# Performance work log

Measured on AMD Instinct MI355X. Metric: run time of the kernel, lower is better.

Reference implementation:

```python
import jax, jax.numpy as jnp
import numpy as np

F_DIM, HID, H, DQ, DV = 1024, 4096, 16, 64, 64
EPS = 1e-6

def layer_norm(x, w, b):
    mu = jnp.mean(x, axis=-1, keepdims=True)
    var = jnp.mean(jnp.square(x - mu), axis=-1, keepdims=True)
    return (x - mu) * jax.lax.rsqrt(var + EPS) * w + b

def setup_inputs() -> dict:
    key = jax.random.key(0)
    ks = jax.random.split(key, 8)
    s = 0.02
    return {
        'x': jax.random.normal(ks[0], (4, 2048, F_DIM), dtype=jnp.float32),
        'ln1_w': jnp.ones((F_DIM,), jnp.float32),
        'ln1_b': jnp.zeros((F_DIM,), jnp.float32),
        'wq_w': jax.random.normal(ks[1], (H * DQ, F_DIM), jnp.float32) * s,
        'wq_b': jnp.zeros((H * DQ,), jnp.float32),
        'wk_w': jax.random.normal(ks[2], (H * DQ, F_DIM), jnp.float32) * s,
        'wk_b': jnp.zeros((H * DQ,), jnp.float32),
        'wv_w': jax.random.normal(ks[3], (H * DV, F_DIM), jnp.float32) * s,
        'wv_b': jnp.zeros((H * DV,), jnp.float32),
        'fc_w': jax.random.normal(ks[4], (F_DIM, H * DV), jnp.float32) * s,
        'fc_b': jnp.zeros((F_DIM,), jnp.float32),
        'ln2_w': jnp.ones((F_DIM,), jnp.float32),
        'ln2_b': jnp.zeros((F_DIM,), jnp.float32),
        'fc1_w': jax.random.normal(ks[5], (HID, F_DIM), jnp.float32) * s,
        'fc1_b': jnp.zeros((HID,), jnp.float32),
        'fc2_w': jax.random.normal(ks[6], (F_DIM, HID), jnp.float32) * s,
        'fc2_b': jnp.zeros((F_DIM,), jnp.float32),
    }

def reference(x, ln1_w, ln1_b, wq_w, wq_b, wk_w, wk_b, wv_w, wv_b,
              fc_w, fc_b, ln2_w, ln2_b, fc1_w, fc1_b, fc2_w, fc2_b):
    B, S, _ = x.shape
    # --- pre-LN multi-head self-attention ---
    h = layer_norm(x, ln1_w, ln1_b)
    q = (h @ wq_w.T + wq_b).reshape(B, S, H, DQ).transpose(0, 2, 1, 3)  # [B,H,S,dq]
    k = (h @ wk_w.T + wk_b).reshape(B, S, H, DQ).transpose(0, 2, 1, 3)
    v = (h @ wv_w.T + wv_b).reshape(B, S, H, DV).transpose(0, 2, 1, 3)
    attn = jax.nn.softmax(jnp.einsum('bhqd,bhkd->bhqk', q, k) / jnp.sqrt(jnp.float32(DQ)), axis=-1)
    out = jnp.einsum('bhqk,bhkd->bhqd', attn, v).transpose(0, 2, 1, 3).reshape(B, S, H * DV)
    x = x + (out @ fc_w.T + fc_b)
    # --- pre-LN residual MLP ---
    h2 = layer_norm(x, ln2_w, ln2_b)
    ff = jax.nn.relu(h2 @ fc1_w.T + fc1_b) @ fc2_w.T + fc2_b
    return x + ff
```

## Files before the change

kernel.cpp:

```cpp
#include <hip/hip_runtime.h>

#define F_DIMC 1024
#define HIDC   4096
#define NH     16
#define SEQ    2048
#define BATCH  4
#define ROWS   (BATCH * SEQ)
#define MEG    (1u << 20)
#define QSCALE 0.18033688011112042f

typedef unsigned short u16t;
typedef __attribute__((ext_vector_type(8))) short short8;
typedef __attribute__((ext_vector_type(4))) float floatx4;
typedef __attribute__((address_space(1))) void gvoid_t;
typedef __attribute__((address_space(3))) void lvoid_t;
#define ASYNC16(g, l) __builtin_amdgcn_global_load_lds((gvoid_t*)(g), (lvoid_t*)(l), 16, 0, 0)

#if __has_builtin(__builtin_amdgcn_exp2f)
#define EXP2(x) __builtin_amdgcn_exp2f(x)
#else
#define EXP2(x) exp2f(x)
#endif

__device__ __forceinline__ u16t f2bf(float f) {
    union { float f; unsigned u; } v; v.f = f;
    unsigned r = v.u + 0x7fffu + ((v.u >> 16) & 1u);
    return (u16t)(r >> 16);
}
__device__ __forceinline__ unsigned fasu(float f) {
    union { float f; unsigned u; } v; v.f = f; return v.u;
}

__global__ __launch_bounds__(256) void ln_kernel(const float* __restrict__ x,
                                                 const float* __restrict__ w,
                                                 const float* __restrict__ b,
                                                 u16t* __restrict__ out) {
    const int row = blockIdx.x;
    const int t = threadIdx.x;
    const float* xp = x + (size_t)row * F_DIMC;

    float4 v = *(const float4*)(xp + t * 4);
    float s  = v.x + v.y + v.z + v.w;
    float ss = v.x * v.x + v.y * v.y + v.z * v.z + v.w * v.w;
    for (int off = 32; off; off >>= 1) {
        s  += __shfl_down(s, off);
        ss += __shfl_down(ss, off);
    }
    __shared__ float red[8];
    const int wid = t >> 6, lid = t & 63;
    if (lid == 0) { red[wid] = s; red[4 + wid] = ss; }
    __syncthreads();
    if (t == 0) {
        float S  = red[0] + red[1] + red[2] + red[3];
        float SS = red[4] + red[5] + red[6] + red[7];
        float mu  = S * (1.0f / F_DIMC);
        float var = SS * (1.0f / F_DIMC) - mu * mu;
        red[0] = mu;
        red[1] = rsqrtf(var + 1e-6f);
    }
    __syncthreads();
    const float mu = red[0], rs = red[1];

    float4 wv = *(const float4*)(w + t * 4);
    float4 bv = *(const float4*)(b + t * 4);
    ushort4 o = make_ushort4(f2bf((v.x - mu) * rs * wv.x + bv.x),
                             f2bf((v.y - mu) * rs * wv.y + bv.y),
                             f2bf((v.z - mu) * rs * wv.z + bv.z),
                             f2bf((v.w - mu) * rs * wv.w + bv.w));
    *(ushort4*)(out + (size_t)row * F_DIMC + t * 4) = o;
}

__global__ __launch_bounds__(256) void wconv_kernel(const float* __restrict__ w0,
        const float* __restrict__ w1, const float* __restrict__ w2,
        const float* __restrict__ w3, const float* __restrict__ w4,
        const float* __restrict__ w5, u16t* __restrict__ dst) {
    const size_t e = ((size_t)blockIdx.x * 256 + threadIdx.x) * 4;
    const float* src; size_t off;
    if      (e < 1 * MEG) { src = w0; off = e; }
    else if (e < 2 * MEG) { src = w1; off = e - 1 * MEG; }
    else if (e < 3 * MEG) { src = w2; off = e - 2 * MEG; }
    else if (e < 4 * MEG) { src = w3; off = e - 3 * MEG; }
    else if (e < 8 * MEG) { src = w4; off = e - 4 * MEG; }
    else                  { src = w5; off = e - 8 * MEG; }
    float4 f = *(const float4*)(src + off);
    *(ushort4*)(dst + e) = make_ushort4(f2bf(f.x), f2bf(f.y), f2bf(f.z), f2bf(f.w));
}

#define DP_PROLOGUE_AND_LOOP(Aq, Wq, Kdim, NBX)                                \
    __shared__ u16t As[2][256 * 64] __attribute__((aligned(16)));              \
    __shared__ u16t Ws[2][128 * 64] __attribute__((aligned(16)));              \
    const int t = threadIdx.x;                                                 \
    const int lane = t & 63;                                                   \
    const int wave = t >> 6;                                                   \
    const int wm = wave >> 1, wn = wave & 1;                                   \
    const int fm = lane & 15, fq = lane >> 4;                                  \
    const int l7 = lane & 7;                                                   \
         \
    const int nwg = gridDim.x;                                                 \
    const int swzb = (blockIdx.x & 7) * (nwg >> 3) + (blockIdx.x >> 3);        \
    const int m0 = (swzb / (NBX)) * 256, n0 = (swzb % (NBX)) * 128;            \
               \
    const u16t* ag[4]; const u16t* wg2[2];                                     \
    int alo[4]; int wlo[2];                                                    \
    _Pragma("unroll")                                                          \
    for (int i = 0; i < 4; ++i) {                                              \
        const int beta = i * 512 + t;                                          \
        const int r = beta >> 3, j = (beta & 7) ^ (r & 7);                     \
        ag[i] = (Aq) + (size_t)(m0 + r) * (Kdim) + j * 8;                      \
        alo[i] = beta * 8;                                                     \
    }                                                                          \
    _Pragma("unroll")                                                          \
    for (int i = 0; i < 2; ++i) {                                              \
        const int beta = i * 512 + t;                                          \
        const int r = beta >> 3, j = (beta & 7) ^ (r & 7);                     \
        wg2[i] = (Wq) + (size_t)(n0 + r) * (Kdim) + j * 8;                     \
        wlo[i] = beta * 8;                                                     \
    }                                                                          \
          \
    int abase[2], bbase[2];                                                    \
    _Pragma("unroll")                                                          \
    for (int ks = 0; ks < 2; ++ks) {                                           \
        const int sw = (ks * 4 + fq) ^ l7;                                     \
        abase[ks] = (wm * 64 + fm) * 64 + sw * 8;                              \
        bbase[ks] = (wn * 64 + fm) * 64 + sw * 8;                              \
    }                                                                          \
    const int NT = (Kdim) / 64;                                                \
                       \
    _Pragma("unroll")                                                          \
    for (int i = 0; i < 4; ++i) ASYNC16(ag[i], &As[0][alo[i]]);                \
    _Pragma("unroll")                                                          \
    for (int i = 0; i < 2; ++i) ASYNC16(wg2[i], &Ws[0][wlo[i]]);               \
    _Pragma("unroll")                                                          \
    for (int i = 0; i < 4; ++i) ASYNC16(ag[i] + 64, &As[1][alo[i]]);           \
    _Pragma("unroll")                                                          \
    for (int i = 0; i < 2; ++i) ASYNC16(wg2[i] + 64, &Ws[1][wlo[i]]);          \
    _Pragma("unroll")                                                          \
    for (int i = 0; i < 4; ++i) ag[i] += 128;                                  \
    _Pragma("unroll")                                                          \
    for (int i = 0; i < 2; ++i) wg2[i] += 128;                                 \
    asm volatile("s_waitcnt vmcnt(6)" ::: "memory");         \
    __builtin_amdgcn_s_barrier();                                              \
    __builtin_amdgcn_sched_barrier(0);                                         \
    floatx4 acc[4][4] = {};                                                    \
    for (int tt = 0; tt < NT; ++tt) {                                          \
        const u16t* Ab = As[tt & 1];                                           \
        const u16t* Wb = Ws[tt & 1];                                           \
                                      \
        short8 fa[4], fb[4];                                                   \
        _Pragma("unroll")                                                      \
        for (int mi = 0; mi < 4; ++mi)                                         \
            fa[mi] = *(const short8*)(Ab + abase[0] + mi * 1024);              \
        _Pragma("unroll")                                                      \
        for (int ni = 0; ni < 4; ++ni)                                         \
            fb[ni] = *(const short8*)(Wb + bbase[0] + ni * 1024);              \
        __builtin_amdgcn_s_setprio(1);                                         \
        _Pragma("unroll")                                                      \
        for (int mi = 0; mi < 4; ++mi)                                         \
            _Pragma("unroll")                                                  \
            for (int ni = 0; ni < 4; ++ni)                                     \
                acc[mi][ni] = __builtin_amdgcn_mfma_f32_16x16x32_bf16(         \
                    fa[mi], fb[ni], acc[mi][ni], 0, 0, 0);                     \
        __builtin_amdgcn_s_setprio(0);                                         \
                     \
        short8 fa1[4], fb1[4];                                                 \
        _Pragma("unroll")                                                      \
        for (int mi = 0; mi < 4; ++mi)                                         \
            fa1[mi] = *(const short8*)(Ab + abase[1] + mi * 1024);             \
        _Pragma("unroll")                                                      \
        for (int ni = 0; ni < 4; ++ni)                                         \
            fb1[ni] = *(const short8*)(Wb + bbase[1] + ni * 1024);             \
        asm volatile("s_waitcnt lgkmcnt(0)" ::: "memory");  \
        __builtin_amdgcn_s_barrier();        \
        __builtin_amdgcn_sched_barrier(0);                                     \
        if (tt + 2 < NT) {                                                     \
            const int pb = tt & 1;           \
            _Pragma("unroll")                                                  \
            for (int i = 0; i < 4; ++i) {                                      \
                ASYNC16(ag[i], &As[pb][alo[i]]); ag[i] += 64;                  \
            }                                                                  \
            _Pragma("unroll")                                                  \
            for (int i = 0; i < 2; ++i) {                                      \
                ASYNC16(wg2[i], &Ws[pb][wlo[i]]); wg2[i] += 64;                \
            }                                                                  \
                  \
            asm volatile("s_waitcnt vmcnt(6)" ::: "memory");                   \
        } else {                                                               \
            asm volatile("s_waitcnt vmcnt(0)" ::: "memory");                   \
        }                                                                      \
        __builtin_amdgcn_s_barrier();                                          \
        __builtin_amdgcn_sched_barrier(0);                                     \
              \
        __builtin_amdgcn_s_setprio(1);                                         \
        _Pragma("unroll")                                                      \
        for (int mi = 0; mi < 4; ++mi)                                         \
            _Pragma("unroll")                                                  \
            for (int ni = 0; ni < 4; ++ni)                                     \
                acc[mi][ni] = __builtin_amdgcn_mfma_f32_16x16x32_bf16(         \
                    fa1[mi], fb1[ni], acc[mi][ni], 0, 0, 0);                   \
        __builtin_amdgcn_s_setprio(0);                                         \
    }

template <bool RELU, bool RES, bool BF16OUT>
__global__ __launch_bounds__(512, 2) void gemm_dp(const u16t* __restrict__ A,
                                                  const u16t* __restrict__ W,
                                                  const float* __restrict__ bias,
                                                  const float* res, void* Cout,
                                                  int N, int K) {
    DP_PROLOGUE_AND_LOOP(A, W, K, N / 128)
    float bl[4];
#pragma unroll
    for (int ni = 0; ni < 4; ++ni) bl[ni] = bias[n0 + wn * 64 + ni * 16 + fm];
#pragma unroll
    for (int mi = 0; mi < 4; ++mi) {
#pragma unroll
        for (int ni = 0; ni < 4; ++ni) {
            const int col = n0 + wn * 64 + ni * 16 + fm;
#pragma unroll
            for (int r = 0; r < 4; ++r) {
                const int row = m0 + wm * 64 + mi * 16 + fq * 4 + r;
                const size_t off = (size_t)row * N + col;
                float c = acc[mi][ni][r] + bl[ni];
                if (RELU) c = fmaxf(c, 0.0f);
                if (RES)  c += res[off];
                if (BF16OUT) ((u16t*)Cout)[off] = f2bf(c);
                else         ((float*)Cout)[off] = c;
            }
        }
    }
}

__global__ __launch_bounds__(512, 2) void gemm_qkv(const u16t* __restrict__ A,
        const u16t* __restrict__ W,
        const float* __restrict__ wq_b, const float* __restrict__ wk_b,
        const float* __restrict__ wv_b,
        u16t* __restrict__ qb, u16t* __restrict__ kb, u16t* __restrict__ vtb) {
    DP_PROLOGUE_AND_LOOP(A, W, F_DIMC, 3072 / 128)
    const int which = n0 >> 10;
    const int nb = n0 & 1023;
    const float* bias = which == 0 ? wq_b : which == 1 ? wk_b : wv_b;
    float bl[4];
#pragma unroll
    for (int ni = 0; ni < 4; ++ni) bl[ni] = bias[nb + wn * 64 + ni * 16 + fm];

    if (which == 2) {
#pragma unroll
        for (int mi = 0; mi < 4; ++mi)
#pragma unroll
            for (int ni = 0; ni < 4; ++ni) {
                const int col = nb + wn * 64 + ni * 16 + fm;
                const int row0 = m0 + wm * 64 + mi * 16 + fq * 4;
                ushort4 pk = make_ushort4(f2bf(acc[mi][ni][0] + bl[ni]),
                                          f2bf(acc[mi][ni][1] + bl[ni]),
                                          f2bf(acc[mi][ni][2] + bl[ni]),
                                          f2bf(acc[mi][ni][3] + bl[ni]));
                *(ushort4*)(vtb + (size_t)col * ROWS + row0) = pk;
            }
    } else {
        u16t* dst = (which == 0) ? qb : kb;
        const float sc = (which == 0) ? QSCALE : 1.0f;
#pragma unroll
        for (int mi = 0; mi < 4; ++mi)
#pragma unroll
            for (int ni = 0; ni < 4; ++ni) {
                const int col = nb + wn * 64 + ni * 16 + fm;
#pragma unroll
                for (int r = 0; r < 4; ++r) {
                    const int row = m0 + wm * 64 + mi * 16 + fq * 4 + r;
                    dst[(size_t)row * F_DIMC + col] = f2bf((acc[mi][ni][r] + bl[ni]) * sc);
                }
            }
    }
}

__global__ __launch_bounds__(256, 4) void attn_mfma(const u16t* __restrict__ qb,
        const u16t* __restrict__ kbuf, const u16t* __restrict__ vtb,
        u16t* __restrict__ ab) {
    __shared__ u16t Kt[2][64 * 64] __attribute__((aligned(16)));
    __shared__ u16t Vs[64 * 64] __attribute__((aligned(16)));
    __shared__ u16t QP[128 * 64] __attribute__((aligned(16)));

    const int t = threadIdx.x;
    const int lane = t & 63;
    const int wave = t >> 6;
    const int l15 = lane & 15, q4 = lane >> 4;
    const int q0 = blockIdx.x * 128;
    const int bh = blockIdx.y;
    const int b = bh >> 4, hh = bh & 15;

#pragma unroll
    for (int c = 0; c < 4; ++c) {
        const int beta = c * 256 + t;
        const int r = beta >> 3, o = (beta & 7) ^ (r & 7);
        ASYNC16(qb + (size_t)(b * SEQ + q0 + r) * F_DIMC + hh * 64 + o * 8,
                QP + beta * 8);
    }
    const u16t* kg = kbuf + (size_t)(b * SEQ) * F_DIMC + hh * 64;
    const u16t* vg = vtb + (size_t)(hh * 64) * ROWS + b * SEQ;

    const int sb0 = t, sb1 = t + 256;
    const int sr0 = sb0 >> 3, so0 = (sb0 & 7) ^ (sr0 & 7);
    const int sr1 = sb1 >> 3, so1 = (sb1 & 7) ^ (sr1 & 7);
    const u16t* kp0 = kg + (size_t)sr0 * F_DIMC + so0 * 8;
    const u16t* kp1 = kg + (size_t)sr1 * F_DIMC + so1 * 8;
    const u16t* vp0 = vg + (size_t)sr0 * ROWS + so0 * 8;
    const u16t* vp1 = vg + (size_t)sr1 * ROWS + so1 * 8;

    ASYNC16(kp0, Kt[0] + sb0 * 8);
    ASYNC16(kp1, Kt[0] + sb1 * 8);
    ASYNC16(vp0, Vs + sb0 * 8);
    ASYNC16(vp1, Vs + sb1 * 8);
    kp0 += 64 * F_DIMC; kp1 += 64 * F_DIMC; vp0 += 64; vp1 += 64;
    __syncthreads();

    short8 fqr[2][2];
#pragma unroll
    for (int mt = 0; mt < 2; ++mt)
#pragma unroll
        for (int ks = 0; ks < 2; ++ks) {
            const int m = wave * 32 + mt * 16 + l15;
            const int oct = ks * 4 + q4;
            fqr[mt][ks] = *(const short8*)(QP + (m * 8 + (oct ^ (m & 7))) * 8);
        }

    short8 ones;
#pragma unroll
    for (int i = 0; i < 8; ++i) ones[i] = (short)0x3F80;

    floatx4 oacc[2][4] = {};
    floatx4 lacc[2] = {};

    for (int it = 0; it < SEQ / 64; ++it) {
        if (it + 1 < SEQ / 64) {
            u16t* kd = Kt[(it + 1) & 1];
            ASYNC16(kp0, kd + sb0 * 8);
            ASYNC16(kp1, kd + sb1 * 8);
            kp0 += 64 * F_DIMC; kp1 += 64 * F_DIMC;
        }
        const u16t* kcur = Kt[it & 1];

        short8 fk[4][2];
#pragma unroll
        for (int nt = 0; nt < 4; ++nt)
#pragma unroll
            for (int ks = 0; ks < 2; ++ks) {
                const int kr = nt * 16 + l15;
                const int oct = ks * 4 + q4;
                fk[nt][ks] = *(const short8*)(kcur + (kr * 8 + (oct ^ (kr & 7))) * 8);
            }
        floatx4 st[2][4] = {};
#pragma unroll
        for (int mt = 0; mt < 2; ++mt)
#pragma unroll
            for (int nt = 0; nt < 4; ++nt) {
                st[mt][nt] = __builtin_amdgcn_mfma_f32_16x16x32_bf16(
                    fk[nt][0], fqr[mt][0], st[mt][nt], 0, 0, 0);
                st[mt][nt] = __builtin_amdgcn_mfma_f32_16x16x32_bf16(
                    fk[nt][1], fqr[mt][1], st[mt][nt], 0, 0, 0);
            }

#pragma unroll
        for (int mt = 0; mt < 2; ++mt)
#pragma unroll
            for (int nt = 0; nt < 4; ++nt) {
                const float p0 = EXP2(st[mt][nt][0]);
                const float p1 = EXP2(st[mt][nt][1]);
                const float p2 = EXP2(st[mt][nt][2]);
                const float p3 = EXP2(st[mt][nt][3]);
                const unsigned lo = __builtin_amdgcn_perm(fasu(p1), fasu(p0), 0x07060302u);
                const unsigned hi = __builtin_amdgcn_perm(fasu(p3), fasu(p2), 0x07060302u);
                const int m = wave * 32 + mt * 16 + l15;
                const int logb = nt * 2 + (q4 >> 1);
                *(uint2*)(QP + (m * 8 + (logb ^ (m & 7))) * 8 + (q4 & 1) * 4) =
                    make_uint2(lo, hi);
            }

        __syncthreads();

        short8 fp[2][2], fv[4][2];
#pragma unroll
        for (int mt = 0; mt < 2; ++mt)
#pragma unroll
            for (int ks = 0; ks < 2; ++ks) {
                const int m = wave * 32 + mt * 16 + l15;
                const int oct = ks * 4 + q4;
                fp[mt][ks] = *(const short8*)(QP + (m * 8 + (oct ^ (m & 7))) * 8);
            }
#pragma unroll
        for (int nd = 0; nd < 4; ++nd)
#pragma unroll
            for (int ks = 0; ks < 2; ++ks) {
                const int d = nd * 16 + l15;
                const int oct = ks * 4 + q4;
                fv[nd][ks] = *(const short8*)(Vs + (d * 8 + (oct ^ (d & 7))) * 8);
            }
#pragma unroll
        for (int mt = 0; mt < 2; ++mt) {
#pragma unroll
            for (int nd = 0; nd < 4; ++nd) {
                oacc[mt][nd] = __builtin_amdgcn_mfma_f32_16x16x32_bf16(
                    fp[mt][0], fv[nd][0], oacc[mt][nd], 0, 0, 0);
                oacc[mt][nd] = __builtin_amdgcn_mfma_f32_16x16x32_bf16(
                    fp[mt][1], fv[nd][1], oacc[mt][nd], 0, 0, 0);
            }
            lacc[mt] = __builtin_amdgcn_mfma_f32_16x16x32_bf16(
                fp[mt][0], ones, lacc[mt], 0, 0, 0);
            lacc[mt] = __builtin_amdgcn_mfma_f32_16x16x32_bf16(
                fp[mt][1], ones, lacc[mt], 0, 0, 0);
        }

        __syncthreads();
        if (it + 1 < SEQ / 64) {
            ASYNC16(vp0, Vs + sb0 * 8);
            ASYNC16(vp1, Vs + sb1 * 8);
            vp0 += 64; vp1 += 64;
        }
    }

#pragma unroll
    for (int mt = 0; mt < 2; ++mt) {
        floatx4 rinv;
#pragma unroll
        for (int r = 0; r < 4; ++r) rinv[r] = 1.0f / lacc[mt][r];
#pragma unroll
        for (int nd = 0; nd < 4; ++nd)
#pragma unroll
            for (int r = 0; r < 4; ++r) {
                const int row = b * SEQ + q0 + wave * 32 + mt * 16 + q4 * 4 + r;
                const int col = hh * 64 + nd * 16 + l15;
                ab[(size_t)row * F_DIMC + col] = f2bf(oacc[mt][nd][r] * rinv[r]);
            }
    }
}

extern "C" void kernel_launch(void* const* d_in, const int* in_sizes, int n_in,
                              void* d_out, int out_size, void* d_ws, size_t ws_size,
                              hipStream_t stream) {
    const float* x     = (const float*)d_in[0];
    const float* ln1_w = (const float*)d_in[1];
    const float* ln1_b = (const float*)d_in[2];
    const float* wq_w  = (const float*)d_in[3];
    const float* wq_b  = (const float*)d_in[4];
    const float* wk_w  = (const float*)d_in[5];
    const float* wk_b  = (const float*)d_in[6];
    const float* wv_w  = (const float*)d_in[7];
    const float* wv_b  = (const float*)d_in[8];
    const float* fc_w  = (const float*)d_in[9];
    const float* fc_b  = (const float*)d_in[10];
    const float* ln2_w = (const float*)d_in[11];
    const float* ln2_b = (const float*)d_in[12];
    const float* fc1_w = (const float*)d_in[13];
    const float* fc1_b = (const float*)d_in[14];
    const float* fc2_w = (const float*)d_in[15];
    const float* fc2_b = (const float*)d_in[16];

    float* out = (float*)d_out;
    u16t*  ws  = (u16t*)d_ws;

    u16t* wbuf = ws;
    u16t* bwqkv = wbuf;
    u16t* bwfc = wbuf + 3 * MEG;
    u16t* bwf1 = wbuf + 4 * MEG;
    u16t* bwf2 = wbuf + 8 * MEG;
    u16t* h    = wbuf + 12 * MEG;
    u16t* qb   = h + 8 * MEG;
    u16t* kb   = qb + 8 * MEG;
    u16t* vtb  = kb + 8 * MEG;
    u16t* ab   = vtb + 8 * MEG;
    u16t* ff   = qb;

    const dim3 blk(256);
    const dim3 blk512(512);
    const int gQKV = (ROWS / 256) * (3072 / 128);
    const int gF   = (ROWS / 256) * (F_DIMC / 128);
    const int gH   = (ROWS / 256) * (HIDC / 128);

    wconv_kernel<<<12 * MEG / 1024, blk, 0, stream>>>(wq_w, wk_w, wv_w, fc_w, fc1_w, fc2_w, wbuf);
    ln_kernel<<<ROWS, blk, 0, stream>>>(x, ln1_w, ln1_b, h);
    gemm_qkv<<<gQKV, blk512, 0, stream>>>(h, bwqkv, wq_b, wk_b, wv_b, qb, kb, vtb);
    attn_mfma<<<dim3(SEQ / 128, BATCH * NH), blk, 0, stream>>>(qb, kb, vtb, ab);
    gemm_dp<false, true, false><<<gF, blk512, 0, stream>>>(ab, bwfc, fc_b, x, out, F_DIMC, F_DIMC);
    ln_kernel<<<ROWS, blk, 0, stream>>>(out, ln2_w, ln2_b, h);
    gemm_dp<true, false, true><<<gH, blk512, 0, stream>>>(h, bwf1, fc1_b, nullptr, ff, HIDC, F_DIMC);
    gemm_dp<false, true, false><<<gF, blk512, 0, stream>>>(ff, bwf2, fc2_b, out, out, F_DIMC, HIDC);
}
```

Measured before the change: 514.7 us.

## Triple-buffer GEMM LDS stages, flip tile to 128x256, drop a barrier

Rewrites the shared GEMM core to use a three-stage LDS ring instead of double buffering. The global-to-LDS prefetch for tile tt+2 is issued at the start of each iteration rather than after a mid-iteration barrier. Both k-halves of the fragments are read up front, which removes one workgroup barrier per k-step. The block tile changes from 256x128 to 128x256 with a 2x4 wave layout, and the block-to-tile mapping changes so consecutive blocks walk along M. The cost is more LDS per block (about 144 KB), which leaves little room under the LDS limit, and a different L2 reuse pattern.

```diff
diff --git a/kernel.cpp b/kernel.cpp
--- a/kernel.cpp
+++ b/kernel.cpp
@@ -86,110 +86,97 @@
     *(ushort4*)(dst + e) = make_ushort4(f2bf(f.x), f2bf(f.y), f2bf(f.z), f2bf(f.w));
 }
 
-#define DP_PROLOGUE_AND_LOOP(Aq, Wq, Kdim, NBX)                                \
-    __shared__ u16t As[2][256 * 64] __attribute__((aligned(16)));              \
-    __shared__ u16t Ws[2][128 * 64] __attribute__((aligned(16)));              \
+#define DP_CORE(Aq, Wq, Kdim)                                                  \
+    __shared__ u16t As[3][128 * 64] __attribute__((aligned(16)));              \
+    __shared__ u16t Bs[3][256 * 64] __attribute__((aligned(16)));              \
     const int t = threadIdx.x;                                                 \
     const int lane = t & 63;                                                   \
     const int wave = t >> 6;                                                   \
-    const int wm = wave >> 1, wn = wave & 1;                                   \
+    const int wm = wave >> 2, wn = wave & 3;                                   \
     const int fm = lane & 15, fq = lane >> 4;                                  \
-    const int l7 = lane & 7;                                                   \
-         \
+        \
     const int nwg = gridDim.x;                                                 \
     const int swzb = (blockIdx.x & 7) * (nwg >> 3) + (blockIdx.x >> 3);        \
-    const int m0 = (swzb / (NBX)) * 256, n0 = (swzb % (NBX)) * 128;            \
-               \
-    const u16t* ag[4]; const u16t* wg2[2];                                     \
-    int alo[4]; int wlo[2];                                                    \
-    _Pragma("unroll")                                                          \
-    for (int i = 0; i < 4; ++i) {                                              \
+    const int m0 = (swzb & 63) * 128;                \
+    const int n0 = (swzb >> 6) * 256;                                          \
+                \
+    const u16t* ag[2]; int alo[2];                                             \
+    _Pragma("unroll")                                                          \
+    for (int i = 0; i < 2; ++i) {                                              \
         const int beta = i * 512 + t;                                          \
         const int r = beta >> 3, j = (beta & 7) ^ (r & 7);                     \
         ag[i] = (Aq) + (size_t)(m0 + r) * (Kdim) + j * 8;                      \
         alo[i] = beta * 8;                                                     \
     }                                                                          \
-    _Pragma("unroll")                                                          \
-    for (int i = 0; i < 2; ++i) {                                              \
+    const u16t* bg[4]; int blo[4];                                             \
+    _Pragma("unroll")                                                          \
+    for (int i = 0; i < 4; ++i) {                                              \
         const int beta = i * 512 + t;                                          \
         const int r = beta >> 3, j = (beta & 7) ^ (r & 7);                     \
-        wg2[i] = (Wq) + (size_t)(n0 + r) * (Kdim) + j * 8;                     \
-        wlo[i] = beta * 8;                                                     \
+        bg[i] = (Wq) + (size_t)(n0 + r) * (Kdim) + j * 8;                      \
+        blo[i] = beta * 8;                                                     \
     }                                                                          \
-          \
-    int abase[2], bbase[2];                                                    \
-    _Pragma("unroll")                                                          \
-    for (int ks = 0; ks < 2; ++ks) {                                           \
-        const int sw = (ks * 4 + fq) ^ l7;                                     \
-        abase[ks] = (wm * 64 + fm) * 64 + sw * 8;                              \
-        bbase[ks] = (wn * 64 + fm) * 64 + sw * 8;                              \
+                \
+    int aoffk[2], boffk[2];                                                    \
+    {                                                                          \
+        const int ra0 = wm * 64 + fm, rb0 = wn * 64 + fm;                      \
+        _Pragma("unroll")                                                      \
+        for (int ks = 0; ks < 2; ++ks) {                                       \
+            aoffk[ks] = ra0 * 64 + ((ks * 4 + fq) ^ (ra0 & 7)) * 8;            \
+            boffk[ks] = rb0 * 64 + ((ks * 4 + fq) ^ (rb0 & 7)) * 8;            \
+        }                                                                      \
     }                                                                          \
     const int NT = (Kdim) / 64;                                                \
                        \
     _Pragma("unroll")                                                          \
-    for (int i = 0; i < 4; ++i) ASYNC16(ag[i], &As[0][alo[i]]);                \
-    _Pragma("unroll")                                                          \
-    for (int i = 0; i < 2; ++i) ASYNC16(wg2[i], &Ws[0][wlo[i]]);               \
-    _Pragma("unroll")                                                          \
-    for (int i = 0; i < 4; ++i) ASYNC16(ag[i] + 64, &As[1][alo[i]]);           \
-    _Pragma("unroll")                                                          \
-    for (int i = 0; i < 2; ++i) ASYNC16(wg2[i] + 64, &Ws[1][wlo[i]]);          \
-    _Pragma("unroll")                                                          \
-    for (int i = 0; i < 4; ++i) ag[i] += 128;                                  \
-    _Pragma("unroll")                                                          \
-    for (int i = 0; i < 2; ++i) wg2[i] += 128;                                 \
+    for (int i = 0; i < 2; ++i) ASYNC16(ag[i], &As[0][alo[i]]);                \
+    _Pragma("unroll")                                                          \
+    for (int i = 0; i < 4; ++i) ASYNC16(bg[i], &Bs[0][blo[i]]);                \
+    _Pragma("unroll")                                                          \
+    for (int i = 0; i < 2; ++i) { ASYNC16(ag[i] + 64, &As[1][alo[i]]); ag[i] += 128; } \
+    _Pragma("unroll")                                                          \
+    for (int i = 0; i < 4; ++i) { ASYNC16(bg[i] + 64, &Bs[1][blo[i]]); bg[i] += 128; } \
     asm volatile("s_waitcnt vmcnt(6)" ::: "memory");         \
     __builtin_amdgcn_s_barrier();                                              \
     __builtin_amdgcn_sched_barrier(0);                                         \
     floatx4 acc[4][4] = {};                                                    \
+    int sc = 0, ss = 2;                                                        \
     for (int tt = 0; tt < NT; ++tt) {                                          \
-        const u16t* Ab = As[tt & 1];                                           \
-        const u16t* Wb = Ws[tt & 1];                                           \
-                                      \
-        short8 fa[4], fb[4];                                                   \
-        _Pragma("unroll")                                                      \
-        for (int mi = 0; mi < 4; ++mi)                                         \
-            fa[mi] = *(const short8*)(Ab + abase[0] + mi * 1024);              \
-        _Pragma("unroll")                                                      \
-        for (int ni = 0; ni < 4; ++ni)                                         \
-            fb[ni] = *(const short8*)(Wb + bbase[0] + ni * 1024);              \
+        const u16t* Ab = As[sc];                                               \
+        const u16t* Bb = Bs[sc];                                               \
+        if (tt + 2 < NT) {                \
+            u16t* la = As[ss]; u16t* lb = Bs[ss];                              \
+            _Pragma("unroll")                                                  \
+            for (int i = 0; i < 2; ++i) { ASYNC16(ag[i], la + alo[i]); ag[i] += 64; } \
+            _Pragma("unroll")                                                  \
+            for (int i = 0; i < 4; ++i) { ASYNC16(bg[i], lb + blo[i]); bg[i] += 64; } \
+        }                                                                      \
+        short8 fb0[4], fa0[4], fb1[4], fa1[4];                                 \
+        _Pragma("unroll")                                                      \
+        for (int ni = 0; ni < 4; ++ni) fb0[ni] = *(const short8*)(Bb + boffk[0] + ni * 1024); \
+        _Pragma("unroll")                                                      \
+        for (int mi = 0; mi < 4; ++mi) fa0[mi] = *(const short8*)(Ab + aoffk[0] + mi * 1024); \
+        _Pragma("unroll")                                                      \
+        for (int ni = 0; ni < 4; ++ni) fb1[ni] = *(const short8*)(Bb + boffk[1] + ni * 1024); \
+        _Pragma("unroll")                                                      \
+        for (int mi = 0; mi < 4; ++mi) fa1[mi] = *(const short8*)(Ab + aoffk[1] + mi * 1024); \
+        asm volatile("s_waitcnt lgkmcnt(8)" ::: "memory");   \
+        __builtin_amdgcn_sched_barrier(0);                                     \
         __builtin_amdgcn_s_setprio(1);                                         \
         _Pragma("unroll")                                                      \
         for (int mi = 0; mi < 4; ++mi)                                         \
             _Pragma("unroll")                                                  \
             for (int ni = 0; ni < 4; ++ni)                                     \
                 acc[mi][ni] = __builtin_amdgcn_mfma_f32_16x16x32_bf16(         \
-                    fa[mi], fb[ni], acc[mi][ni], 0, 0, 0);                     \
+                    fa0[mi], fb0[ni], acc[mi][ni], 0, 0, 0);                   \
         __builtin_amdgcn_s_setprio(0);                                         \
-                     \
-        short8 fa1[4], fb1[4];                                                 \
-        _Pragma("unroll")                                                      \
-        for (int mi = 0; mi < 4; ++mi)                                         \
-            fa1[mi] = *(const short8*)(Ab + abase[1] + mi * 1024);             \
-        _Pragma("unroll")                                                      \
-        for (int ni = 0; ni < 4; ++ni)                                         \
-            fb1[ni] = *(const short8*)(Wb + bbase[1] + ni * 1024);             \
-        asm volatile("s_waitcnt lgkmcnt(0)" ::: "memory");  \
-        __builtin_amdgcn_s_barrier();        \
+        asm volatile("s_waitcnt lgkmcnt(0)" ::: "memory");   \
         __builtin_amdgcn_sched_barrier(0);                                     \
-        if (tt + 2 < NT) {                                                     \
-            const int pb = tt & 1;           \
-            _Pragma("unroll")                                                  \
-            for (int i = 0; i < 4; ++i) {                                      \
-                ASYNC16(ag[i], &As[pb][alo[i]]); ag[i] += 64;                  \
-            }                                                                  \
-            _Pragma("unroll")                                                  \
-            for (int i = 0; i < 2; ++i) {                                      \
-                ASYNC16(wg2[i], &Ws[pb][wlo[i]]); wg2[i] += 64;                \
-            }                                                                  \
-                  \
-            asm volatile("s_waitcnt vmcnt(6)" ::: "memory");                   \
-        } else {                                                               \
-            asm volatile("s_waitcnt vmcnt(0)" ::: "memory");                   \
-        }                                                                      \
+                                       \
+        if (tt + 2 < NT) { asm volatile("s_waitcnt vmcnt(6)" ::: "memory"); }  \
+        else             { asm volatile("s_waitcnt vmcnt(0)" ::: "memory"); }  \
         __builtin_amdgcn_s_barrier();                                          \
         __builtin_amdgcn_sched_barrier(0);                                     \
-              \
         __builtin_amdgcn_s_setprio(1);                                         \
         _Pragma("unroll")                                                      \
         for (int mi = 0; mi < 4; ++mi)                                         \
@@ -198,6 +185,8 @@
                 acc[mi][ni] = __builtin_amdgcn_mfma_f32_16x16x32_bf16(         \
                     fa1[mi], fb1[ni], acc[mi][ni], 0, 0, 0);                   \
         __builtin_amdgcn_s_setprio(0);                                         \
+        sc = sc == 2 ? 0 : sc + 1;                                             \
+        ss = ss == 2 ? 0 : ss + 1;                                             \
     }
 
 template <bool RELU, bool RES, bool BF16OUT>
@@ -206,7 +195,7 @@
                                                   const float* __restrict__ bias,
                                                   const float* res, void* Cout,
                                                   int N, int K) {
-    DP_PROLOGUE_AND_LOOP(A, W, K, N / 128)
+    DP_CORE(A, W, K)
     float bl[4];
 #pragma unroll
     for (int ni = 0; ni < 4; ++ni) bl[ni] = bias[n0 + wn * 64 + ni * 16 + fm];
@@ -234,7 +223,7 @@
         const float* __restrict__ wq_b, const float* __restrict__ wk_b,
         const float* __restrict__ wv_b,
         u16t* __restrict__ qb, u16t* __restrict__ kb, u16t* __restrict__ vtb) {
-    DP_PROLOGUE_AND_LOOP(A, W, F_DIMC, 3072 / 128)
+    DP_CORE(A, W, F_DIMC)
     const int which = n0 >> 10;
     const int nb = n0 & 1023;
     const float* bias = which == 0 ? wq_b : which == 1 ? wk_b : wv_b;
@@ -257,7 +246,7 @@
             }
     } else {
         u16t* dst = (which == 0) ? qb : kb;
-        const float sc = (which == 0) ? QSCALE : 1.0f;
+        const float sc2 = (which == 0) ? QSCALE : 1.0f;
 #pragma unroll
         for (int mi = 0; mi < 4; ++mi)
 #pragma unroll
@@ -266,7 +255,7 @@
 #pragma unroll
                 for (int r = 0; r < 4; ++r) {
                     const int row = m0 + wm * 64 + mi * 16 + fq * 4 + r;
-                    dst[(size_t)row * F_DIMC + col] = f2bf((acc[mi][ni][r] + bl[ni]) * sc);
+                    dst[(size_t)row * F_DIMC + col] = f2bf((acc[mi][ni][r] + bl[ni]) * sc2);
                 }
             }
     }
@@ -470,9 +459,9 @@
 
     const dim3 blk(256);
     const dim3 blk512(512);
-    const int gQKV = (ROWS / 256) * (3072 / 128);
-    const int gF   = (ROWS / 256) * (F_DIMC / 128);
-    const int gH   = (ROWS / 256) * (HIDC / 128);
+    const int gQKV = 64 * (3072 / 256);
+    const int gF   = 64 * (F_DIMC / 256);
+    const int gH   = 64 * (HIDC / 256);
 
     wconv_kernel<<<12 * MEG / 1024, blk, 0, stream>>>(wq_w, wk_w, wv_w, fc_w, fc1_w, fc2_w, wbuf);
     ln_kernel<<<ROWS, blk, 0, stream>>>(x, ln1_w, ln1_b, h);
```

Measured after the change: 565.0 us. +9.8%, slower.
